# Kernel tuning notes

Measured on AMD Instinct MI355X. Metric: run time of the kernel, lower is better.

The kernel has to match this reference:

```python
import jax, jax.numpy as jnp
import numpy as np

H = 64          # nheads
NH = 8          # lru_dim // nheads (per-head state dim, must be even)
LRU_DIM = 512
HIDDEN = 512
BATCH = 8
T = 4096
MAX_PHASE = 6.28
R_MIN, R_MAX = 0.9, 0.999


def setup_inputs() -> dict:
    key = jax.random.key(0)
    ks = jax.random.split(key, 8)
    input_sequence = jax.random.normal(ks[0], (BATCH, 1, HIDDEN, 1, T), dtype=jnp.float32)
    # theta_init: log(uniform(0, max_phase)), shape (lru_dim//2, 1)
    theta_log = jnp.log(jax.random.uniform(ks[1], (LRU_DIM // 2, 1), maxval=MAX_PHASE))
    # ortho_mat_init(lru_dim, N)
    P = jax.random.normal(ks[2], (LRU_DIM, NH)) / jnp.sqrt(NH + LRU_DIM)
    # mat_init(lru_dim, hidden_dim)
    B = jax.random.normal(ks[3], (LRU_DIM, HIDDEN)) / jnp.sqrt(HIDDEN + LRU_DIM)
    # mat_init(hidden_dim, lru_dim)
    C = jax.random.normal(ks[4], (HIDDEN, LRU_DIM)) / jnp.sqrt(HIDDEN + LRU_DIM)
    D = jax.random.normal(ks[5], (HIDDEN,))
    # nu_log_init: log(-log r) interpolated by uniform
    u1 = jax.random.uniform(ks[6], (H,))
    gamma_log = jnp.log(-jnp.log(R_MAX)) + u1 * (jnp.log(-jnp.log(R_MIN)) - jnp.log(-jnp.log(R_MAX)))
    return dict(input_sequence=input_sequence, theta_log=theta_log, P=P, B=B, C=C, D=D,
                gamma_log=gamma_log)


def _mix_sequence(gamma, thetas, Us):
    """Single head. gamma: scalar, thetas: (N/2,), Us: (T, B, N) -> (T, B, N)."""
    def binf(a, b):
        g_i, th_i, acc_i = a
        g_j, th_j, acc_j = b
        # rotate-half (RoPE-style) of accumulated state
        rot = jnp.stack([-acc_i[..., 1::2], acc_i[..., 0::2]], axis=-1).reshape(acc_i.shape)
        theta = jnp.repeat(th_j[..., None], 2, axis=-1).reshape(th_j.shape[:-1] + (th_j.shape[-1] * 2,))
        sin = jnp.sin(theta)[..., None, :]  # (..., 1, N)
        cos = jnp.cos(theta)[..., None, :]
        acc = g_j[..., None, None] * (cos * acc_i + sin * rot)
        return (g_i * g_j, th_i + th_j, acc + acc_j)

    Tlen = Us.shape[0]
    gammas = jnp.repeat(gamma[None], Tlen, axis=0)          # (T,)
    Rs = jnp.repeat(thetas[None, :], Tlen, axis=0)          # (T, N/2)
    _, _, res = jax.lax.associative_scan(binf, (gammas, Rs, Us))
    return res


def reference(input_sequence, theta_log, P, B, C, D, gamma_log):
    x = input_sequence[:, 0, :, 0].transpose(0, 2, 1)       # (B, T, hidden)
    bsz, Tlen, _ = x.shape
    thetas = jnp.exp(theta_log.reshape(H, NH // 2))          # (H, N/2)
    Pm = P.reshape(H, NH, NH)
    Bm = B.reshape(H, NH, HIDDEN)
    gamma = jnp.exp(-jnp.exp(gamma_log))                     # (H,)
    # trace(B B^T) per head == sum of squares
    trace_per_head = jnp.sum(Bm * Bm, axis=(1, 2))
    norm = jnp.sqrt((1.0 - gamma ** 2) / trace_per_head)
    B_norm = norm[:, None, None] * Bm                        # (H, N, hidden)
    # orthogonalize P via matrix exponential of skew-symmetric part
    Pm = jax.vmap(jax.scipy.linalg.expm)(Pm - Pm.transpose(0, 2, 1))  # (H, N, N)
    Us = jnp.einsum('HnD,BTD->HTBn', B_norm, x)              # project inputs per head
    Us = jnp.einsum('HnN,HTBn->HTBN', Pm.transpose(0, 2, 1), Us)
    y = jax.vmap(_mix_sequence)(gamma, thetas, Us)           # (H, T, B, N)
    y = jnp.einsum('HNn,HTBN->HTBn', Pm, y)
    y = y.transpose(2, 1, 0, 3).reshape(bsz, Tlen, -1)       # (B, T, lru_dim)
    y = jnp.einsum('Dn,BTn->BTD', C, y) + D * x
    return y[0]                                              # (T, hidden)
```

## Files before the change

kernel.cpp:

```cpp
#include <hip/hip_runtime.h>
#include <math.h>

#define NHEADS   64
#define TLEN     4096
#define CHUNK    16
#define NCHUNK   256

typedef unsigned short u16;
typedef unsigned int   u32;
typedef __attribute__((ext_vector_type(8))) short bf16x8;
typedef __attribute__((ext_vector_type(4))) float f32x4;

__device__ __forceinline__ u16 f2bf(float x) {
    u32 u = __float_as_uint(x);
    u32 r = (u + 0x7FFFu + ((u >> 16) & 1u)) >> 16;
    return (u16)r;
}
__device__ __forceinline__ float bf2f(u16 h) { return __uint_as_float(((u32)h) << 16); }
__device__ __forceinline__ u16 f2bf_trunc(float x) { return (u16)(__float_as_uint(x) >> 16); }


__global__ void k_pre(const float* __restrict__ X, u16* __restrict__ XT,
                      const float* __restrict__ P,
                      const float* __restrict__ Bmat,
                      const float* __restrict__ theta_log,
                      const float* __restrict__ gamma_log,
                      float* __restrict__ ws) {
    const int tid = threadIdx.x;
    if (blockIdx.x < 512) {
        __shared__ float Xs[64][65];
        const int t0 = (blockIdx.x & 63) * 64, d0 = (blockIdx.x >> 6) * 64;
        {
            const int dr = tid >> 4, tc = (tid & 15) * 4;
            #pragma unroll
            for (int it = 0; it < 4; ++it) {
                const int dd = it*16 + dr;
                float4 v = *reinterpret_cast<const float4*>(X + (size_t)(d0 + dd)*4096 + t0 + tc);
                Xs[dd][tc] = v.x; Xs[dd][tc+1] = v.y; Xs[dd][tc+2] = v.z; Xs[dd][tc+3] = v.w;
            }
        }
        __syncthreads();
        const int tr = tid >> 2, ds = (tid & 3) * 16;
        u32 hb[8], lb[8];
        #pragma unroll
        for (int j = 0; j < 16; j += 2) {
            float a = Xs[ds + j][tr], b = Xs[ds + j + 1][tr];
            u16 ha = f2bf(a), la = f2bf(a - bf2f(ha));
            u16 hbb = f2bf(b), lbb = f2bf(b - bf2f(hbb));
            hb[j >> 1] = (u32)ha | ((u32)hbb << 16);
            lb[j >> 1] = (u32)la | ((u32)lbb << 16);
        }
        u16* orow = XT + (size_t)(t0 + tr)*1024 + d0 + ds;
        uint4 h0; h0.x = hb[0]; h0.y = hb[1]; h0.z = hb[2]; h0.w = hb[3];
        uint4 h1; h1.x = hb[4]; h1.y = hb[5]; h1.z = hb[6]; h1.w = hb[7];
        uint4 l0; l0.x = lb[0]; l0.y = lb[1]; l0.z = lb[2]; l0.w = lb[3];
        uint4 l1; l1.x = lb[4]; l1.y = lb[5]; l1.z = lb[6]; l1.w = lb[7];
        *reinterpret_cast<uint4*>(orow)       = h0;
        *reinterpret_cast<uint4*>(orow + 8)   = h1;
        *reinterpret_cast<uint4*>(orow + 512) = l0;
        *reinterpret_cast<uint4*>(orow + 520) = l1;
        return;
    }
    __shared__ double As[8][8];
    __shared__ double Rs[8][8];
    __shared__ double red[256];
    __shared__ int sh_s;
    const int h = blockIdx.x - 512;
    const int i = (tid & 63) >> 3, j = tid & 7;
    const bool act = tid < 64;

    if (act)
        As[i][j] = (double)P[(h*8 + i)*8 + j] - (double)P[(h*8 + j)*8 + i];

    const float* Bh = Bmat + h*8*512;
    double ss = 0.0;
    #pragma unroll
    for (int q = 0; q < 16; ++q) { float v = Bh[q*256 + tid]; ss += (double)v * (double)v; }
    red[tid] = ss;
    __syncthreads();

    if (tid == 0) {
        double nrm = 0.0;
        for (int r = 0; r < 8; ++r) {
            double rs = 0.0;
            for (int c = 0; c < 8; ++c) rs += fabs(As[r][c]);
            nrm = fmax(nrm, rs);
        }
        int s = 0;
        while (nrm > 0.25 && s < 40) { nrm *= 0.5; ++s; }
        sh_s = s;
        double tr = 0.0;
        for (int q = 0; q < 256; ++q) tr += red[q];
        double ed = exp((double)gamma_log[h]);
        double g  = exp(-ed);
        ws[4096 + h] = (float)g;
        ws[4416 + h] = (float)sqrt((1.0 - g*g) / tr);
    }
    if (tid < 4) ws[4160 + h*4 + tid] = expf(theta_log[h*4 + tid]);
    __syncthreads();

    const int NT = 13;
    if (act) {
        const double sc = ldexp(1.0, -sh_s);
        As[i][j] *= sc;
        Rs[i][j] = (i == j ? 1.0 : 0.0) + As[i][j] / (double)NT;
    }
    __syncthreads();
    for (int k = NT - 1; k >= 1; --k) {
        double t = 0.0;
        if (act) {
            #pragma unroll
            for (int m = 0; m < 8; ++m) t += As[i][m] * Rs[m][j];
        }
        __syncthreads();
        if (act) Rs[i][j] = (i == j ? 1.0 : 0.0) + t / (double)k;
        __syncthreads();
    }
    const int nsq = sh_s;
    for (int q = 0; q < nsq; ++q) {
        double t = 0.0;
        if (act) {
            #pragma unroll
            for (int m = 0; m < 8; ++m) t += Rs[i][m] * Rs[m][j];
        }
        __syncthreads();
        if (act) Rs[i][j] = t;
        __syncthreads();
    }
    if (act) ws[h*64 + i*8 + j] = (float)Rs[i][j];
}

__global__ void k_proj(const float* __restrict__ Bmat,
                       const float* __restrict__ C,
                       const float* __restrict__ ws_ro,
                       u16* __restrict__ W1pk,
                       u16* __restrict__ CEpk) {
    const int gid = blockIdx.x * 256 + threadIdx.x;
    if (gid < 512*512) {
        const int k = gid >> 9, d = gid & 511;
        const int h = k >> 3, N = k & 7;
        const float* Pm = ws_ro + h*64 + N*8;
        const float nrm = ws_ro[4416 + h];
        float acc = 0.f;
        #pragma unroll
        for (int n = 0; n < 8; ++n) acc += Pm[n] * Bmat[(h*8 + n)*512 + d];
        acc *= nrm;
        u16 hi = f2bf(acc), lo = f2bf(acc - bf2f(hi));
        W1pk[k*1024 + d] = hi;
        W1pk[k*1024 + 512 + d] = lo;
    } else {
        const int g2 = gid - 512*512;
        const int e = g2 >> 9, k = g2 & 511;
        const int h = k >> 3, N = k & 7;
        const float* Pm = ws_ro + h*64 + N*8;
        float acc = 0.f;
        #pragma unroll
        for (int n = 0; n < 8; ++n) acc += Pm[n] * C[e*512 + h*8 + n];
        u16 hi = f2bf(acc), lo = f2bf(acc - bf2f(hi));
        CEpk[e*1024 + k] = hi;
        CEpk[e*1024 + 512 + k] = lo;
    }
}

#define MFMA_BF16(A_, B_, C_) __builtin_amdgcn_mfma_f32_16x16x32_bf16(A_, B_, C_, 0, 0, 0)
template<int MODE>
__global__ __launch_bounds__(256, 2) void k_gemm(const u16* __restrict__ Apk,
                                                 const float* __restrict__ Af,
                                                 const u16* __restrict__ Bpk,
                                                 float* __restrict__ Cout,
                                                 const u16* __restrict__ XT,
                                                 const float* __restrict__ Dvec,
                                                 const float* __restrict__ wsro,
                                                 float* __restrict__ E,
                                                 const float* __restrict__ S,
                                                 const float* __restrict__ TAB) {
    __shared__ char smem[73728];
    float* Ut = (float*)smem;

    const int tid = threadIdx.x;
    const int bid = blockIdx.x;
    const int tile = (bid & 7) * 64 + (bid >> 3);
    const int mt = tile >> 3, nt = tile & 7;
    const int m0 = mt * 64, n0 = nt * 64;
    const int lane = tid & 63, wid = tid >> 6;
    const int wm = wid >> 1, wn = wid & 1;
    const int lr = lane & 15, lc = lane >> 4;
    const int sr = tid >> 2, ss = (tid & 3) * 16;

    f32x4 acc00 = {0.f,0.f,0.f,0.f}, acc01 = acc00, acc10 = acc00, acc11 = acc00;

    const int tA = m0 + sr;
    const int cA = tA >> 4, iA = tA & 15;
    const u16* Brow = Bpk + (size_t)(n0 + sr)*1024 + ss;
    const u16* Arow = (MODE == 0) ? (Apk + (size_t)tA*1024 + ss) : (const u16*)0;
    const float* Urow = (MODE == 1) ? (Af + (size_t)tA*512 + ss) : (const float*)0;

    float4 rb0, rb1, rb2, rb3;
    float4 ra0, ra1, ra2, ra3;
    float4 ru[4], rtb[4], rsv[4];

    auto LOADREGS = [&](int k0) {
        rb0 = *reinterpret_cast<const float4*>(Brow + k0);
        rb1 = *reinterpret_cast<const float4*>(Brow + k0 + 8);
        rb2 = *reinterpret_cast<const float4*>(Brow + 512 + k0);
        rb3 = *reinterpret_cast<const float4*>(Brow + 512 + k0 + 8);
        if constexpr (MODE == 0) {
            ra0 = *reinterpret_cast<const float4*>(Arow + k0);
            ra1 = *reinterpret_cast<const float4*>(Arow + k0 + 8);
            ra2 = *reinterpret_cast<const float4*>(Arow + 512 + k0);
            ra3 = *reinterpret_cast<const float4*>(Arow + 512 + k0 + 8);
        } else {
            const int p0 = (k0 + ss) >> 1;
            #pragma unroll
            for (int j = 0; j < 4; ++j) {
                ru[j]  = *reinterpret_cast<const float4*>(Urow + k0 + 4*j);
                rtb[j] = *reinterpret_cast<const float4*>(TAB + ((size_t)iA*256 + p0 + 2*j)*2);
                rsv[j] = *reinterpret_cast<const float4*>(S + (size_t)cA*512 + 2*p0 + 4*j);
            }
        }
    };
    auto STORE = [&](u16* Ah, u16* Al, u16* Bh, u16* Bl) {
        if constexpr (MODE == 0) {
            *reinterpret_cast<float4*>(&Ah[sr*72 + ss])     = ra0;
            *reinterpret_cast<float4*>(&Ah[sr*72 + ss + 8]) = ra1;
            *reinterpret_cast<float4*>(&Al[sr*72 + ss])     = ra2;
            *reinterpret_cast<float4*>(&Al[sr*72 + ss + 8]) = ra3;
        } else {
            #pragma unroll
            for (int j = 0; j < 4; ++j) {
                float4 u = ru[j], tb = rtb[j], sv = rsv[j];
                u.x += tb.x*sv.x - tb.y*sv.y;
                u.y += tb.y*sv.x + tb.x*sv.y;
                u.z += tb.z*sv.z - tb.w*sv.w;
                u.w += tb.w*sv.z + tb.z*sv.w;
                u16 hx = f2bf(u.x), hy = f2bf(u.y), hz = f2bf(u.z), hw = f2bf(u.w);
                u16 lx = f2bf_trunc(u.x - bf2f(hx)), ly = f2bf_trunc(u.y - bf2f(hy));
                u16 lz = f2bf_trunc(u.z - bf2f(hz)), lw = f2bf_trunc(u.w - bf2f(hw));
                uint2 wh; wh.x = (u32)hx | ((u32)hy << 16); wh.y = (u32)hz | ((u32)hw << 16);
                uint2 wl; wl.x = (u32)lx | ((u32)ly << 16); wl.y = (u32)lz | ((u32)lw << 16);
                *reinterpret_cast<uint2*>(&Ah[sr*72 + ss + 4*j]) = wh;
                *reinterpret_cast<uint2*>(&Al[sr*72 + ss + 4*j]) = wl;
            }
        }
        *reinterpret_cast<float4*>(&Bh[sr*72 + ss])     = rb0;
        *reinterpret_cast<float4*>(&Bh[sr*72 + ss + 8]) = rb1;
        *reinterpret_cast<float4*>(&Bl[sr*72 + ss])     = rb2;
        *reinterpret_cast<float4*>(&Bl[sr*72 + ss + 8]) = rb3;
    };
    auto MFMAS = [&](const u16* Ah, const u16* Al, const u16* Bh, const u16* Bl) {
        #pragma unroll
        for (int kk = 0; kk < 2; ++kk) {
            const int ko = kk*32 + lc*8;
            const int ra0i = (wm*32 + lr)*72 + ko,  ra1i = ra0i + 16*72;
            const int rb0i = (wn*32 + lr)*72 + ko,  rb1i = rb0i + 16*72;
            bf16x8 fah0 = *reinterpret_cast<const bf16x8*>(&Ah[ra0i]);
            bf16x8 fah1 = *reinterpret_cast<const bf16x8*>(&Ah[ra1i]);
            bf16x8 fal0 = *reinterpret_cast<const bf16x8*>(&Al[ra0i]);
            bf16x8 fal1 = *reinterpret_cast<const bf16x8*>(&Al[ra1i]);
            bf16x8 fbh0 = *reinterpret_cast<const bf16x8*>(&Bh[rb0i]);
            bf16x8 fbh1 = *reinterpret_cast<const bf16x8*>(&Bh[rb1i]);
            bf16x8 fbl0 = *reinterpret_cast<const bf16x8*>(&Bl[rb0i]);
            bf16x8 fbl1 = *reinterpret_cast<const bf16x8*>(&Bl[rb1i]);
            acc00 = MFMA_BF16(fah0, fbl0, acc00);
            acc00 = MFMA_BF16(fal0, fbh0, acc00);
            acc00 = MFMA_BF16(fah0, fbh0, acc00);
            acc01 = MFMA_BF16(fah0, fbl1, acc01);
            acc01 = MFMA_BF16(fal0, fbh1, acc01);
            acc01 = MFMA_BF16(fah0, fbh1, acc01);
            acc10 = MFMA_BF16(fah1, fbl0, acc10);
            acc10 = MFMA_BF16(fal1, fbh0, acc10);
            acc10 = MFMA_BF16(fah1, fbh0, acc10);
            acc11 = MFMA_BF16(fah1, fbl1, acc11);
            acc11 = MFMA_BF16(fal1, fbh1, acc11);
            acc11 = MFMA_BF16(fah1, fbh1, acc11);
        }
    };

    u16* buf0 = (u16*)smem;
    u16* buf1 = (u16*)(smem + 36864);

    LOADREGS(0);
    STORE(buf0, buf0 + 4608, buf0 + 9216, buf0 + 13824);
    __syncthreads();

    #pragma unroll
    for (int s = 0; s < 8; ++s) {
        u16* bp = (s & 1) ? buf1 : buf0;
        u16* bq = (s & 1) ? buf0 : buf1;
        if (s < 7) LOADREGS((s + 1) * 64);
        MFMAS(bp, bp + 4608, bp + 9216, bp + 13824);
        if (s < 7) STORE(bq, bq + 4608, bq + 9216, bq + 13824);
        __syncthreads();
    }

    if constexpr (MODE == 0) {
        #pragma unroll
        for (int im = 0; im < 2; ++im) {
            #pragma unroll
            for (int in = 0; in < 2; ++in) {
                f32x4 v = (im == 0) ? (in == 0 ? acc00 : acc01)
                                    : (in == 0 ? acc10 : acc11);
                const int row0 = wm*32 + im*16 + lc*4;
                const int col  = wn*32 + in*16 + lr;
                #pragma unroll
                for (int rg = 0; rg < 4; ++rg)
                    Ut[(row0 + rg)*72 + col] = v[rg];
            }
        }
        __syncthreads();
        if (tid < 128) {
            const int cc = tid >> 5, pp = tid & 31;
            const int pg = nt*32 + pp;
            const float th = wsro[4160 + pg];
            const float g  = wsro[4096 + (pg >> 2)];
            const float cs = cosf(th), sn = sinf(th);
            float h0 = 0.f, h1 = 0.f;
            float* col = Ut + (cc*16)*72 + 2*pp;
            #pragma unroll
            for (int i = 0; i < CHUNK; ++i) {
                float a = col[i*72], b = col[i*72 + 1];
                float n0v = g*(cs*h0 - sn*h1) + a;
                float n1v = g*(sn*h0 + cs*h1) + b;
                col[i*72] = n0v; col[i*72 + 1] = n1v;
                h0 = n0v; h1 = n1v;
            }
            E[(size_t)(mt*4 + cc)*512 + 2*pg]     = h0;
            E[(size_t)(mt*4 + cc)*512 + 2*pg + 1] = h1;
        }
        __syncthreads();
        const int row = tid >> 2, cseg = (tid & 3) * 16;
        #pragma unroll
        for (int j = 0; j < 4; ++j) {
            float4 v = *reinterpret_cast<const float4*>(&Ut[row*72 + cseg + 4*j]);
            *reinterpret_cast<float4*>(Cout + (size_t)(m0 + row)*512 + n0 + cseg + 4*j) = v;
        }
    } else {
        #pragma unroll
        for (int im = 0; im < 2; ++im) {
            #pragma unroll
            for (int in = 0; in < 2; ++in) {
                f32x4 v = (im == 0) ? (in == 0 ? acc00 : acc01)
                                    : (in == 0 ? acc10 : acc11);
                const int row0 = m0 + wm*32 + im*16 + lc*4;
                const int col  = n0 + wn*32 + in*16 + lr;
                const float dv = Dvec[col];
                #pragma unroll
                for (int rg = 0; rg < 4; ++rg) {
                    const int t = row0 + rg;
                    float xv = bf2f(XT[(size_t)t*1024 + col]) + bf2f(XT[(size_t)t*1024 + 512 + col]);
                    Cout[(size_t)t*512 + col] = v[rg] + dv*xv;
                }
            }
        }
    }
}

__global__ void k_carry(const float* __restrict__ E, float* __restrict__ S,
                        float* __restrict__ TAB,
                        const float* __restrict__ theta_log,
                        const float* __restrict__ gamma_log) {
    const int w = threadIdx.x >> 6, l = threadIdx.x & 63;
    const int p = blockIdx.x*4 + w;
    const double th = exp((double)theta_log[p]);
    const double ed = exp((double)gamma_log[p >> 2]);

    if (l < CHUNK) {
        double a = (double)(l + 1) * th;
        double g = exp(-(double)(l + 1) * ed);
        TAB[((size_t)l*256 + p)*2 + 0] = (float)(g * cos(a));
        TAB[((size_t)l*256 + p)*2 + 1] = (float)(g * sin(a));
    }

    const double a16 = 16.0*th, g16 = exp(-16.0*ed);
    const float Lc = (float)(g16*cos(a16)), Ls = (float)(g16*sin(a16));

    const float* Ep = E + 2*p;
    float2 e0 = *reinterpret_cast<const float2*>(Ep + (size_t)(4*l + 0)*512);
    float2 e1 = *reinterpret_cast<const float2*>(Ep + (size_t)(4*l + 1)*512);
    float2 e2 = *reinterpret_cast<const float2*>(Ep + (size_t)(4*l + 2)*512);
    float2 e3 = *reinterpret_cast<const float2*>(Ep + (size_t)(4*l + 3)*512);

    float2 v = e0;
    v = make_float2(Lc*v.x - Ls*v.y + e1.x, Ls*v.x + Lc*v.y + e1.y);
    v = make_float2(Lc*v.x - Ls*v.y + e2.x, Ls*v.x + Lc*v.y + e2.y);
    v = make_float2(Lc*v.x - Ls*v.y + e3.x, Ls*v.x + Lc*v.y + e3.y);

    #pragma unroll
    for (int d = 0; d < 6; ++d) {
        const int sh = 1 << d;
        const double aa = 64.0 * (double)sh * th;
        const double gg = exp(-64.0 * (double)sh * ed);
        const float Mc = (float)(gg*cos(aa)), Ms = (float)(gg*sin(aa));
        float px = __shfl_up(v.x, sh, 64);
        float py = __shfl_up(v.y, sh, 64);
        if (l >= sh) {
            v.x += Mc*px - Ms*py;
            v.y += Ms*px + Mc*py;
        }
    }

    float sx = __shfl_up(v.x, 1, 64), sy = __shfl_up(v.y, 1, 64);
    float2 s = (l == 0) ? make_float2(0.f, 0.f) : make_float2(sx, sy);
    float* Sp = S + 2*p;
    *reinterpret_cast<float2*>(Sp + (size_t)(4*l + 0)*512) = s;
    s = make_float2(Lc*s.x - Ls*s.y + e0.x, Ls*s.x + Lc*s.y + e0.y);
    *reinterpret_cast<float2*>(Sp + (size_t)(4*l + 1)*512) = s;
    s = make_float2(Lc*s.x - Ls*s.y + e1.x, Ls*s.x + Lc*s.y + e1.y);
    *reinterpret_cast<float2*>(Sp + (size_t)(4*l + 2)*512) = s;
    s = make_float2(Lc*s.x - Ls*s.y + e2.x, Ls*s.x + Lc*s.y + e2.y);
    *reinterpret_cast<float2*>(Sp + (size_t)(4*l + 3)*512) = s;
}

extern "C" void kernel_launch(void* const* d_in, const int* in_sizes, int n_in,
                              void* d_out, int out_size, void* d_ws, size_t ws_size,
                              hipStream_t stream) {
    const float* X  = (const float*)d_in[0];
    const float* th = (const float*)d_in[1];
    const float* P  = (const float*)d_in[2];
    const float* Bm = (const float*)d_in[3];
    const float* C  = (const float*)d_in[4];
    const float* Dv = (const float*)d_in[5];
    const float* gl = (const float*)d_in[6];
    char* wsb = (char*)d_ws;
    float* ws   = (float*)wsb;
    u16*   W1pk = (u16*)(wsb + 32768);
    u16*   CEpk = (u16*)(wsb + 1081344);
    u16*   XTpk = (u16*)(wsb + 2129920);
    float* U    = (float*)(wsb + 10518528);
    float* E    = (float*)(wsb + 18907136);
    float* S    = (float*)(wsb + 19431424);
    float* TAB  = (float*)(wsb + 19955712);
    float* out  = (float*)d_out;

    k_pre<<<576, 256, 0, stream>>>(X, XTpk, P, Bm, th, gl, ws);
    k_proj<<<2048, 256, 0, stream>>>(Bm, C, ws, W1pk, CEpk);
    k_gemm<0><<<512, 256, 0, stream>>>(XTpk, (const float*)0, W1pk, U, XTpk, Dv, ws, E, S, TAB);
    k_carry<<<64, 256, 0, stream>>>(E, S, TAB, th, gl);
    k_gemm<1><<<512, 256, 0, stream>>>((const u16*)0, U, CEpk, out, XTpk, Dv, ws, E, S, TAB);
}
```

Baseline: 148.2 us.

## Fuse X transpose/split into GEMM load and merge projection into k_pre

Removes the separate pass that transposed X and stored it as split bf16 hi/lo in workspace. The first GEMM now reads fp32 X directly in its native (D,T) layout and does the hi/lo split while staging to shared memory, and the epilogue reads X directly for the D*x term. The k_proj kernel is folded into k_pre, one block per head, which computes the P-projected B and C weights from shared memory. This cuts two launches and the XT round-trip through memory, but the GEMM tile loads are now strided across D rows, and k_pre runs on only 64 blocks.

```diff
diff --git a/kernel.cpp b/kernel.cpp
--- a/kernel.cpp
+++ b/kernel.cpp
@@ -20,52 +20,23 @@
 __device__ __forceinline__ u16 f2bf_trunc(float x) { return (u16)(__float_as_uint(x) >> 16); }
 
 
-__global__ void k_pre(const float* __restrict__ X, u16* __restrict__ XT,
-                      const float* __restrict__ P,
+__global__ void k_pre(const float* __restrict__ P,
                       const float* __restrict__ Bmat,
+                      const float* __restrict__ C,
                       const float* __restrict__ theta_log,
                       const float* __restrict__ gamma_log,
-                      float* __restrict__ ws) {
-    const int tid = threadIdx.x;
-    if (blockIdx.x < 512) {
-        __shared__ float Xs[64][65];
-        const int t0 = (blockIdx.x & 63) * 64, d0 = (blockIdx.x >> 6) * 64;
-        {
-            const int dr = tid >> 4, tc = (tid & 15) * 4;
-            #pragma unroll
-            for (int it = 0; it < 4; ++it) {
-                const int dd = it*16 + dr;
-                float4 v = *reinterpret_cast<const float4*>(X + (size_t)(d0 + dd)*4096 + t0 + tc);
-                Xs[dd][tc] = v.x; Xs[dd][tc+1] = v.y; Xs[dd][tc+2] = v.z; Xs[dd][tc+3] = v.w;
-            }
-        }
-        __syncthreads();
-        const int tr = tid >> 2, ds = (tid & 3) * 16;
-        u32 hb[8], lb[8];
-        #pragma unroll
-        for (int j = 0; j < 16; j += 2) {
-            float a = Xs[ds + j][tr], b = Xs[ds + j + 1][tr];
-            u16 ha = f2bf(a), la = f2bf(a - bf2f(ha));
-            u16 hbb = f2bf(b), lbb = f2bf(b - bf2f(hbb));
-            hb[j >> 1] = (u32)ha | ((u32)hbb << 16);
-            lb[j >> 1] = (u32)la | ((u32)lbb << 16);
-        }
-        u16* orow = XT + (size_t)(t0 + tr)*1024 + d0 + ds;
-        uint4 h0; h0.x = hb[0]; h0.y = hb[1]; h0.z = hb[2]; h0.w = hb[3];
-        uint4 h1; h1.x = hb[4]; h1.y = hb[5]; h1.z = hb[6]; h1.w = hb[7];
-        uint4 l0; l0.x = lb[0]; l0.y = lb[1]; l0.z = lb[2]; l0.w = lb[3];
-        uint4 l1; l1.x = lb[4]; l1.y = lb[5]; l1.z = lb[6]; l1.w = lb[7];
-        *reinterpret_cast<uint4*>(orow)       = h0;
-        *reinterpret_cast<uint4*>(orow + 8)   = h1;
-        *reinterpret_cast<uint4*>(orow + 512) = l0;
-        *reinterpret_cast<uint4*>(orow + 520) = l1;
-        return;
-    }
+                      float* __restrict__ ws,
+                      u16* __restrict__ W1pk,
+                      u16* __restrict__ CEpk) {
+    __shared__ float  Bsh[8*512];
+    __shared__ float  Pf[64];
     __shared__ double As[8][8];
     __shared__ double Rs[8][8];
     __shared__ double red[256];
-    __shared__ int sh_s;
-    const int h = blockIdx.x - 512;
+    __shared__ int    sh_s;
+    __shared__ float  sh_nrm;
+    const int h = blockIdx.x;
+    const int tid = threadIdx.x;
     const int i = (tid & 63) >> 3, j = tid & 7;
     const bool act = tid < 64;
 
@@ -75,7 +46,11 @@
     const float* Bh = Bmat + h*8*512;
     double ss = 0.0;
     #pragma unroll
-    for (int q = 0; q < 16; ++q) { float v = Bh[q*256 + tid]; ss += (double)v * (double)v; }
+    for (int q = 0; q < 16; ++q) {
+        float v = Bh[q*256 + tid];
+        Bsh[q*256 + tid] = v;
+        ss += (double)v * (double)v;
+    }
     red[tid] = ss;
     __syncthreads();
 
@@ -94,7 +69,9 @@
         double ed = exp((double)gamma_log[h]);
         double g  = exp(-ed);
         ws[4096 + h] = (float)g;
-        ws[4416 + h] = (float)sqrt((1.0 - g*g) / tr);
+        float nf = (float)sqrt((1.0 - g*g) / tr);
+        ws[4416 + h] = nf;
+        sh_nrm = nf;
     }
     if (tid < 4) ws[4160 + h*4 + tid] = expf(theta_log[h*4 + tid]);
     __syncthreads();
@@ -127,48 +104,60 @@
         if (act) Rs[i][j] = t;
         __syncthreads();
     }
-    if (act) ws[h*64 + i*8 + j] = (float)Rs[i][j];
-}
-
-__global__ void k_proj(const float* __restrict__ Bmat,
-                       const float* __restrict__ C,
-                       const float* __restrict__ ws_ro,
-                       u16* __restrict__ W1pk,
-                       u16* __restrict__ CEpk) {
-    const int gid = blockIdx.x * 256 + threadIdx.x;
-    if (gid < 512*512) {
-        const int k = gid >> 9, d = gid & 511;
-        const int h = k >> 3, N = k & 7;
-        const float* Pm = ws_ro + h*64 + N*8;
-        const float nrm = ws_ro[4416 + h];
-        float acc = 0.f;
-        #pragma unroll
-        for (int n = 0; n < 8; ++n) acc += Pm[n] * Bmat[(h*8 + n)*512 + d];
-        acc *= nrm;
-        u16 hi = f2bf(acc), lo = f2bf(acc - bf2f(hi));
-        W1pk[k*1024 + d] = hi;
-        W1pk[k*1024 + 512 + d] = lo;
-    } else {
-        const int g2 = gid - 512*512;
-        const int e = g2 >> 9, k = g2 & 511;
-        const int h = k >> 3, N = k & 7;
-        const float* Pm = ws_ro + h*64 + N*8;
-        float acc = 0.f;
-        #pragma unroll
-        for (int n = 0; n < 8; ++n) acc += Pm[n] * C[e*512 + h*8 + n];
-        u16 hi = f2bf(acc), lo = f2bf(acc - bf2f(hi));
-        CEpk[e*1024 + k] = hi;
-        CEpk[e*1024 + 512 + k] = lo;
+    if (act) Pf[i*8 + j] = (float)Rs[i][j];
+    __syncthreads();
+
+    const float nrmf = sh_nrm;
+    {
+        const int d0 = 2*tid;
+        #pragma unroll
+        for (int N = 0; N < 8; ++N) {
+            float a0 = 0.f, a1 = 0.f;
+            #pragma unroll
+            for (int n = 0; n < 8; ++n) {
+                const float pm = Pf[N*8 + n];
+                a0 += pm * Bsh[n*512 + d0];
+                a1 += pm * Bsh[n*512 + d0 + 1];
+            }
+            a0 *= nrmf; a1 *= nrmf;
+            u16 h0 = f2bf(a0), h1 = f2bf(a1);
+            u16 l0 = f2bf_trunc(a0 - bf2f(h0)), l1 = f2bf_trunc(a1 - bf2f(h1));
+            u16* base = W1pk + (size_t)(8*h + N)*1024;
+            *reinterpret_cast<u32*>(base + d0)       = (u32)h0 | ((u32)h1 << 16);
+            *reinterpret_cast<u32*>(base + 512 + d0) = (u32)l0 | ((u32)l1 << 16);
+        }
+    }
+    #pragma unroll
+    for (int ee = 0; ee < 2; ++ee) {
+        const int e = ee*256 + tid;
+        float4 c0 = *reinterpret_cast<const float4*>(C + (size_t)e*512 + 8*h);
+        float4 c1 = *reinterpret_cast<const float4*>(C + (size_t)e*512 + 8*h + 4);
+        float cv[8] = {c0.x, c0.y, c0.z, c0.w, c1.x, c1.y, c1.z, c1.w};
+        u16 hv[8], lv[8];
+        #pragma unroll
+        for (int N = 0; N < 8; ++N) {
+            float acc = 0.f;
+            #pragma unroll
+            for (int n = 0; n < 8; ++n) acc += Pf[N*8 + n] * cv[n];
+            hv[N] = f2bf(acc);
+            lv[N] = f2bf_trunc(acc - bf2f(hv[N]));
+        }
+        u16* base = CEpk + (size_t)e*1024 + 8*h;
+        uint4 wh; wh.x = (u32)hv[0] | ((u32)hv[1] << 16); wh.y = (u32)hv[2] | ((u32)hv[3] << 16);
+                  wh.z = (u32)hv[4] | ((u32)hv[5] << 16); wh.w = (u32)hv[6] | ((u32)hv[7] << 16);
+        uint4 wl; wl.x = (u32)lv[0] | ((u32)lv[1] << 16); wl.y = (u32)lv[2] | ((u32)lv[3] << 16);
+                  wl.z = (u32)lv[4] | ((u32)lv[5] << 16); wl.w = (u32)lv[6] | ((u32)lv[7] << 16);
+        *reinterpret_cast<uint4*>(base)       = wh;
+        *reinterpret_cast<uint4*>(base + 512) = wl;
     }
 }
 
 #define MFMA_BF16(A_, B_, C_) __builtin_amdgcn_mfma_f32_16x16x32_bf16(A_, B_, C_, 0, 0, 0)
 template<int MODE>
-__global__ __launch_bounds__(256, 2) void k_gemm(const u16* __restrict__ Apk,
+__global__ __launch_bounds__(256, 2) void k_gemm(const float* __restrict__ Xf,
                                                  const float* __restrict__ Af,
                                                  const u16* __restrict__ Bpk,
                                                  float* __restrict__ Cout,
-                                                 const u16* __restrict__ XT,
                                                  const float* __restrict__ Dvec,
                                                  const float* __restrict__ wsro,
                                                  float* __restrict__ E,
@@ -186,17 +175,18 @@
     const int wm = wid >> 1, wn = wid & 1;
     const int lr = lane & 15, lc = lane >> 4;
     const int sr = tid >> 2, ss = (tid & 3) * 16;
+    const int tgrp4 = (tid & 15) * 4;
+    const int dgrp4 = (tid >> 4) * 4;
 
     f32x4 acc00 = {0.f,0.f,0.f,0.f}, acc01 = acc00, acc10 = acc00, acc11 = acc00;
 
     const int tA = m0 + sr;
     const int cA = tA >> 4, iA = tA & 15;
     const u16* Brow = Bpk + (size_t)(n0 + sr)*1024 + ss;
-    const u16* Arow = (MODE == 0) ? (Apk + (size_t)tA*1024 + ss) : (const u16*)0;
     const float* Urow = (MODE == 1) ? (Af + (size_t)tA*512 + ss) : (const float*)0;
 
     float4 rb0, rb1, rb2, rb3;
-    float4 ra0, ra1, ra2, ra3;
+    float4 rx0, rx1, rx2, rx3;
     float4 ru[4], rtb[4], rsv[4];
 
     auto LOADREGS = [&](int k0) {
@@ -205,10 +195,11 @@
         rb2 = *reinterpret_cast<const float4*>(Brow + 512 + k0);
         rb3 = *reinterpret_cast<const float4*>(Brow + 512 + k0 + 8);
         if constexpr (MODE == 0) {
-            ra0 = *reinterpret_cast<const float4*>(Arow + k0);
-            ra1 = *reinterpret_cast<const float4*>(Arow + k0 + 8);
-            ra2 = *reinterpret_cast<const float4*>(Arow + 512 + k0);
-            ra3 = *reinterpret_cast<const float4*>(Arow + 512 + k0 + 8);
+            const float* Xc = Xf + (size_t)(k0 + dgrp4)*4096 + m0 + tgrp4;
+            rx0 = *reinterpret_cast<const float4*>(Xc);
+            rx1 = *reinterpret_cast<const float4*>(Xc + 4096);
+            rx2 = *reinterpret_cast<const float4*>(Xc + 8192);
+            rx3 = *reinterpret_cast<const float4*>(Xc + 12288);
         } else {
             const int p0 = (k0 + ss) >> 1;
             #pragma unroll
@@ -221,10 +212,21 @@
     };
     auto STORE = [&](u16* Ah, u16* Al, u16* Bh, u16* Bl) {
         if constexpr (MODE == 0) {
-            *reinterpret_cast<float4*>(&Ah[sr*72 + ss])     = ra0;
-            *reinterpret_cast<float4*>(&Ah[sr*72 + ss + 8]) = ra1;
-            *reinterpret_cast<float4*>(&Al[sr*72 + ss])     = ra2;
-            *reinterpret_cast<float4*>(&Al[sr*72 + ss + 8]) = ra3;
+            const float* r0 = &rx0.x;
+            const float* r1 = &rx1.x;
+            const float* r2 = &rx2.x;
+            const float* r3 = &rx3.x;
+            #pragma unroll
+            for (int tt = 0; tt < 4; ++tt) {
+                float a0 = r0[tt], a1 = r1[tt], a2 = r2[tt], a3 = r3[tt];
+                u16 h0 = f2bf(a0), h1 = f2bf(a1), h2 = f2bf(a2), h3 = f2bf(a3);
+                u16 l0 = f2bf_trunc(a0 - bf2f(h0)), l1 = f2bf_trunc(a1 - bf2f(h1));
+                u16 l2 = f2bf_trunc(a2 - bf2f(h2)), l3 = f2bf_trunc(a3 - bf2f(h3));
+                uint2 wh; wh.x = (u32)h0 | ((u32)h1 << 16); wh.y = (u32)h2 | ((u32)h3 << 16);
+                uint2 wl; wl.x = (u32)l0 | ((u32)l1 << 16); wl.y = (u32)l2 | ((u32)l3 << 16);
+                *reinterpret_cast<uint2*>(&Ah[(tgrp4 + tt)*72 + dgrp4]) = wh;
+                *reinterpret_cast<uint2*>(&Al[(tgrp4 + tt)*72 + dgrp4]) = wl;
+            }
         } else {
             #pragma unroll
             for (int j = 0; j < 4; ++j) {
@@ -344,12 +346,11 @@
                 const int row0 = m0 + wm*32 + im*16 + lc*4;
                 const int col  = n0 + wn*32 + in*16 + lr;
                 const float dv = Dvec[col];
+                float4 xv = *reinterpret_cast<const float4*>(Xf + (size_t)col*4096 + row0);
+                const float* xp = &xv.x;
                 #pragma unroll
-                for (int rg = 0; rg < 4; ++rg) {
-                    const int t = row0 + rg;
-                    float xv = bf2f(XT[(size_t)t*1024 + col]) + bf2f(XT[(size_t)t*1024 + 512 + col]);
-                    Cout[(size_t)t*512 + col] = v[rg] + dv*xv;
-                }
+                for (int rg = 0; rg < 4; ++rg)
+                    Cout[(size_t)(row0 + rg)*512 + col] = v[rg] + dv * xp[rg];
             }
         }
     }
@@ -425,16 +426,14 @@
     float* ws   = (float*)wsb;
     u16*   W1pk = (u16*)(wsb + 32768);
     u16*   CEpk = (u16*)(wsb + 1081344);
-    u16*   XTpk = (u16*)(wsb + 2129920);
     float* U    = (float*)(wsb + 10518528);
     float* E    = (float*)(wsb + 18907136);
     float* S    = (float*)(wsb + 19431424);
     float* TAB  = (float*)(wsb + 19955712);
     float* out  = (float*)d_out;
 
-    k_pre<<<576, 256, 0, stream>>>(X, XTpk, P, Bm, th, gl, ws);
-    k_proj<<<2048, 256, 0, stream>>>(Bm, C, ws, W1pk, CEpk);
-    k_gemm<0><<<512, 256, 0, stream>>>(XTpk, (const float*)0, W1pk, U, XTpk, Dv, ws, E, S, TAB);
+    k_pre<<<NHEADS, 256, 0, stream>>>(P, Bm, C, th, gl, ws, W1pk, CEpk);
+    k_gemm<0><<<512, 256, 0, stream>>>(X, (const float*)0, W1pk, U, Dv, ws, E, S, TAB);
     k_carry<<<64, 256, 0, stream>>>(E, S, TAB, th, gl);
-    k_gemm<1><<<512, 256, 0, stream>>>((const u16*)0, U, CEpk, out, XTpk, Dv, ws, E, S, TAB);
+    k_gemm<1><<<512, 256, 0, stream>>>(X, U, CEpk, out, Dv, ws, E, S, TAB);
 }
```

Result: slower. 154.5 us (+4.2%).
